# Kernel optimization log

Measured on AMD Instinct MI355X. Metric: run time of the kernel, lower is better.

The kernel has to match this reference:

```python
import jax, jax.numpy as jnp
import numpy as np

NUM_BANDS = 400
LATENT = 8
NUM_LAYERS = 2
K = 10  # num_selected_bands
FF = 128
EPS = 1e-5


def _xavier(key, shape):
    fan_in, fan_out = shape[-1], shape[-2] if len(shape) >= 2 else shape[-1]
    lim = float(np.sqrt(6.0 / (fan_in + fan_out)))
    return jax.random.uniform(key, shape, jnp.float32, -lim, lim)


def setup_inputs() -> dict:
    key = jax.random.key(0)
    ks = jax.random.split(key, 20)
    B, H, W = 1, 256, 256
    d = {
        "x": jax.random.normal(ks[0], (B, NUM_BANDS, H, W), jnp.float32),
        "x_original": jax.random.normal(ks[1], (B, NUM_BANDS, H, W), jnp.float32),
        "pos": _xavier(ks[2], (1, NUM_BANDS)),
        "band_importance": jnp.zeros((NUM_BANDS,), jnp.float32),
        # per-layer transformer params stacked on a leading layer axis
        "Wv": _xavier(ks[3], (NUM_LAYERS, NUM_BANDS, NUM_BANDS)),
        "bv": jnp.zeros((NUM_LAYERS, NUM_BANDS), jnp.float32),
        "Wo": _xavier(ks[4], (NUM_LAYERS, NUM_BANDS, NUM_BANDS)),
        "bo": jnp.zeros((NUM_LAYERS, NUM_BANDS), jnp.float32),
        "ln1_w": jnp.ones((NUM_LAYERS, NUM_BANDS), jnp.float32),
        "ln1_b": jnp.zeros((NUM_LAYERS, NUM_BANDS), jnp.float32),
        "W1": _xavier(ks[5], (NUM_LAYERS, FF, NUM_BANDS)),
        "b1": jnp.zeros((NUM_LAYERS, FF), jnp.float32),
        "W2": _xavier(ks[6], (NUM_LAYERS, NUM_BANDS, FF)),
        "b2": jnp.zeros((NUM_LAYERS, NUM_BANDS), jnp.float32),
        "ln2_w": jnp.ones((NUM_LAYERS, NUM_BANDS), jnp.float32),
        "ln2_b": jnp.zeros((NUM_LAYERS, NUM_BANDS), jnp.float32),
        # lightweight encoder: K -> LATENT -> LATENT
        "We1": _xavier(ks[7], (LATENT, K)),
        "be1": jnp.zeros((LATENT,), jnp.float32),
        "We2": _xavier(ks[8], (LATENT, LATENT)),
        "be2": jnp.zeros((LATENT,), jnp.float32),
        # decoder: LATENT -> LATENT -> NUM_BANDS
        "Wd1": _xavier(ks[9], (LATENT, LATENT)),
        "bd1": jnp.zeros((LATENT,), jnp.float32),
        "Wd2": _xavier(ks[10], (NUM_BANDS, LATENT)),
        "bd2": jnp.zeros((NUM_BANDS,), jnp.float32),
    }
    return d


def _layer_norm(h, w, b):
    mu = jnp.mean(h, axis=-1, keepdims=True)
    var = jnp.mean(jnp.square(h - mu), axis=-1, keepdims=True)
    return (h - mu) * jax.lax.rsqrt(var + EPS) * w + b


def reference(x, x_original, pos, band_importance, Wv, bv, Wo, bo, ln1_w, ln1_b,
              W1, b1, W2, b2, ln2_w, ln2_b, We1, be1, We2, be2, Wd1, bd1, Wd2, bd2):
    B, C, H, W = x.shape
    # [B,C,H,W] -> [B*H*W, C] tokens; learnable positional encoding over bands
    tok = jnp.transpose(x, (0, 2, 3, 1)).reshape(-1, C) + pos

    # TransformerEncoder (post-norm, relu). Seq-first convention => seq_len=1,
    # so softmax over the single score is 1 and self_attn(x) == out_proj(v_proj(x)).
    h = tok
    for i in range(NUM_LAYERS):
        attn = (h @ Wv[i].T + bv[i]) @ Wo[i].T + bo[i]
        h = _layer_norm(h + attn, ln1_w[i], ln1_b[i])
        ff = jax.nn.relu(h @ W1[i].T + b1[i]) @ W2[i].T + b2[i]
        h = _layer_norm(h + ff, ln2_w[i], ln2_b[i])

    attention_scores = h * jax.nn.sigmoid(band_importance)  # [N, C]
    top_v, top_i = jax.lax.top_k(attention_scores, K)       # sorted desc by value
    order = jnp.argsort(top_i, axis=1)
    sorted_idx = jnp.take_along_axis(top_i, order, axis=1)
    sorted_val = jnp.take_along_axis(top_v, order, axis=1)

    orig = jnp.transpose(x_original, (0, 2, 3, 1)).reshape(-1, C)
    selected_bands1 = jnp.take_along_axis(orig, sorted_idx, axis=1)  # [N, K]
    selected = selected_bands1 * sorted_val

    enc = jax.nn.relu(selected @ We1.T + be1) @ We2.T + be2          # [N, LATENT]
    dec = jax.nn.relu(enc @ Wd1.T + bd1) @ Wd2.T + bd2               # [N, C]
    reconstructed = jnp.transpose(dec.reshape(B, H, W, C), (0, 3, 1, 2))
    return reconstructed, sorted_idx, attention_scores, selected_bands1
```

## Files before the change

### kernel.cpp

```cpp
#include <hip/hip_runtime.h>
#include <hip/hip_bf16.h>
#include <math.h>

#define NBANDS 400
#define NPIX   65536
#define FFW    128
#define KSEL   10
#define TOK    16
#define HS     403
#define FS     131

typedef double f64x4 __attribute__((ext_vector_type(4)));
#define MFMA64(a,b,c) __builtin_amdgcn_mfma_f64_16x16x4f64((a),(b),(c),0,0,0)

static constexpr size_t WSB_WVOT = 0;
static constexpr size_t WSB_BVO  = 2560000;
static constexpr size_t WSB_SIG  = 2566400;
static constexpr size_t WSB_W1T  = 2569600;
static constexpr size_t WSB_W2T  = 2979200;
static constexpr size_t WS_NEED  = 3388800;

static constexpr size_t REC_OFF = 0;
static constexpr size_t IDX_OFF = 26214400;
static constexpr size_t SCO_OFF = IDX_OFF + 655360;
static constexpr size_t SEL_OFF = SCO_OFF + 26214400;
static constexpr int    OUT_EXPECT = 53739520;


__global__ void prep_wvot(const float* __restrict__ Wv, const float* __restrict__ Wo,
                          double* __restrict__ WvoT) {
    int b = blockIdx.x;
    int l = b / 400, j = b - l * 400;
    int k = threadIdx.x;
    if (k >= 400) return;
    const float* wo = Wo + l * 160000 + j * 400;
    const float* wv = Wv + l * 160000;
    double acc = 0.0;
    #pragma unroll 4
    for (int m = 0; m < 400; ++m)
        acc += (double)wo[m] * (double)wv[m * 400 + k];
    WvoT[l * 160000 + k * 400 + j] = acc;
}

__global__ void prep_transpose(const float* __restrict__ W1, const float* __restrict__ W2,
                               float* __restrict__ W1T, float* __restrict__ W2T) {
    int idx = blockIdx.x * blockDim.x + threadIdx.x;
    if (idx < 2 * FFW * NBANDS) {
        int l = idx / (FFW * NBANDS); int r = idx - l * (FFW * NBANDS);
        int jf = r / NBANDS; int k = r - jf * NBANDS;
        W1T[l * FFW * NBANDS + k * FFW + jf] = W1[idx];
        int j = r / FFW; int kf = r - j * FFW;
        W2T[l * FFW * NBANDS + kf * NBANDS + j] = W2[idx];
    }
}

__global__ void prep_small(const float* __restrict__ Wo, const float* __restrict__ bv,
                           const float* __restrict__ bo, const float* __restrict__ bi,
                           double* __restrict__ bvo, double* __restrict__ sigd) {
    int g = blockIdx.x * blockDim.x + threadIdx.x;
    if (g < 800) {
        int l = g / 400;
        const float* wo = Wo + l * 160000 + (g - l * 400) * 400;
        const float* bb = bv + l * 400;
        double acc = (double)bo[g];
        for (int m = 0; m < 400; ++m) acc += (double)wo[m] * (double)bb[m];
        bvo[g] = acc;
    } else if (g < 1200) {
        int c = g - 800;
        sigd[c] = 1.0 / (1.0 + exp(-(double)bi[c]));
    }
}

__global__ void sentinel_kernel(float* out, float v) {
    out[blockIdx.x * 256 + threadIdx.x] = v;
}


__device__ inline void layer_norm_inplace(double* __restrict__ h, double* __restrict__ red,
                                          const float* __restrict__ w, const float* __restrict__ b,
                                          int tid) {
    {
        int t = tid >> 5, q = tid & 31;
        double s = 0.0, ss = 0.0;
        for (int j = q; j < NBANDS; j += 32) {
            double v = h[t * HS + j]; s += v; ss += v * v;
        }
        #pragma unroll
        for (int m = 1; m < 32; m <<= 1) {
            s  += __shfl_xor(s, m, 64);
            ss += __shfl_xor(ss, m, 64);
        }
        if (q == 0) { red[t * 2] = s; red[t * 2 + 1] = ss; }
    }
    __syncthreads();
    for (int idx = tid; idx < TOK * NBANDS; idx += 512) {
        int t = idx / NBANDS, j = idx - t * NBANDS;
        double mu  = red[t * 2] / 400.0;
        double var = red[t * 2 + 1] / 400.0 - mu * mu;
        double rs  = 1.0 / sqrt(var + 1e-5);
        h[t * HS + j] = (h[t * HS + j] - mu) * rs * (double)w[j] + (double)b[j];
    }
    __syncthreads();
}

__global__ __launch_bounds__(512) void hbsm_main(
    const float* __restrict__ x, const float* __restrict__ xo,
    const float* __restrict__ pos,
    const float* __restrict__ ln1w, const float* __restrict__ ln1b,
    const float* __restrict__ b1,   const float* __restrict__ b2,
    const float* __restrict__ ln2w, const float* __restrict__ ln2b,
    const float* __restrict__ We1,  const float* __restrict__ be1,
    const float* __restrict__ We2,  const float* __restrict__ be2,
    const float* __restrict__ Wd1,  const float* __restrict__ bd1,
    const float* __restrict__ Wd2,  const float* __restrict__ bd2,
    const double* __restrict__ WvoT, const double* __restrict__ bvo,
    const double* __restrict__ sigd,
    const float* __restrict__ W1Tf,  const float* __restrict__ W2Tf,
    float* __restrict__ out)
{
    extern __shared__ double smem[];
    double* h    = smem;
    double* f    = h + TOK * HS;
    double* red  = f + TOK * FS;
    double* lval = red + 64;
    double* sigs = lval + 160;
    float*  d1s  = (float*)(sigs + 400);
    int*    lidx = (int*)(d1s + 144);

    const int tid  = threadIdx.x;
    const int p0   = blockIdx.x * TOK;
    const int lane = tid & 63;
    const int wv   = tid >> 6;
    const int rA   = lane & 15;
    const int kq   = lane >> 4;

    int rowm[4], colm[4];
    {
        f64x4 z = {0.0, 0.0, 0.0, 0.0};
        f64x4 pr = MFMA64(0.25 * (double)rA, 1.0, z);
        f64x4 pc = MFMA64(0.25, (double)rA, z);
        #pragma unroll
        for (int i = 0; i < 4; ++i) {
            rowm[i] = ((int)(pr[i] + 0.5)) & 15;
            colm[i] = ((int)(pc[i] + 0.5)) & 15;
        }
    }

    for (int i = tid; i < NBANDS; i += 512) sigs[i] = sigd[i];
    for (int i = tid; i < TOK * NBANDS; i += 512) {
        int t = i & 15, c = i >> 4;
        float xv = __builtin_nontemporal_load(&x[(size_t)c * NPIX + p0 + t]);
        h[t * HS + c] = (double)xv + (double)pos[c];
    }
    __syncthreads();

    const double* hA = h + rA * HS;
    const int c0 = wv * 16 + rA, c1 = c0 + 128, c2 = c0 + 256;
    const int ct = 384 + rA;
    const bool xtraA = (wv == 0);
    const bool xtraF = (wv == 4);

    for (int l = 0; l < 2; ++l) {
        {
            const double* WT  = WvoT + l * 160000;
            const double* bb0 = bvo + l * 400;
            f64x4 a0={0,0,0,0}, a1={0,0,0,0}, a2={0,0,0,0}, a3={0,0,0,0};
            #pragma unroll 2
            for (int k0 = 0; k0 < NBANDS; k0 += 4) {
                double av = hA[k0 + kq];
                const double* wrow = WT + (size_t)(k0 + kq) * 400;
                a0 = MFMA64(av, wrow[c0], a0);
                a1 = MFMA64(av, wrow[c1], a1);
                a2 = MFMA64(av, wrow[c2], a2);
                if (xtraA) a3 = MFMA64(av, wrow[ct], a3);
            }
            __syncthreads();
            #pragma unroll
            for (int i = 0; i < 4; ++i) {
                int r  = rowm[i];
                int j0 = wv * 16 + colm[i], j1 = j0 + 128, j2 = j0 + 256;
                h[r * HS + j0] += a0[i] + bb0[j0];
                h[r * HS + j1] += a1[i] + bb0[j1];
                h[r * HS + j2] += a2[i] + bb0[j2];
                if (xtraA) {
                    int jt = 384 + colm[i];
                    h[r * HS + jt] += a3[i] + bb0[jt];
                }
            }
            __syncthreads();
        }
        layer_norm_inplace(h, red, ln1w + l * 400, ln1b + l * 400, tid);

        {
            const float* WT  = W1Tf + (size_t)l * 51200;
            const float* bb1 = b1 + l * FFW;
            const int cf = wv * 16 + rA;
            f64x4 e0 = {0,0,0,0};
            #pragma unroll 2
            for (int k0 = 0; k0 < NBANDS; k0 += 4) {
                double av = hA[k0 + kq];
                double b = (double)WT[(size_t)(k0 + kq) * FFW + cf];
                e0 = MFMA64(av, b, e0);
            }
            #pragma unroll
            for (int i = 0; i < 4; ++i) {
                int r  = rowm[i];
                int jf = wv * 16 + colm[i];
                double v0 = e0[i] + (double)bb1[jf];
                f[r * FS + jf] = v0 > 0.0 ? v0 : 0.0;
            }
            __syncthreads();
        }

        {
            const float* WT  = W2Tf + (size_t)l * 51200;
            const float* bb2 = b2 + l * 400;
            const double* fA = f + rA * FS;
            f64x4 a0={0,0,0,0}, a1={0,0,0,0}, a2={0,0,0,0}, a3={0,0,0,0};
            #pragma unroll 2
            for (int k0 = 0; k0 < FFW; k0 += 4) {
                double av = fA[k0 + kq];
                const float* wrow = WT + (size_t)(k0 + kq) * 400;
                a0 = MFMA64(av, (double)wrow[c0], a0);
                a1 = MFMA64(av, (double)wrow[c1], a1);
                a2 = MFMA64(av, (double)wrow[c2], a2);
                if (xtraF) a3 = MFMA64(av, (double)wrow[ct], a3);
            }
            #pragma unroll
            for (int i = 0; i < 4; ++i) {
                int r  = rowm[i];
                int j0 = wv * 16 + colm[i], j1 = j0 + 128, j2 = j0 + 256;
                h[r * HS + j0] += a0[i] + (double)bb2[j0];
                h[r * HS + j1] += a1[i] + (double)bb2[j1];
                h[r * HS + j2] += a2[i] + (double)bb2[j2];
                if (xtraF) {
                    int jt = 384 + colm[i];
                    h[r * HS + jt] += a3[i] + (double)bb2[jt];
                }
            }
            __syncthreads();
        }
        layer_norm_inplace(h, red, ln2w + l * 400, ln2b + l * 400, tid);
    }

    for (int idx = tid; idx < TOK * NBANDS; idx += 512) {
        int t = idx / NBANDS, c = idx - t * NBANDS;
        __builtin_nontemporal_store((float)(h[t * HS + c] * sigs[c]),
                                    &out[SCO_OFF + (size_t)(p0 + t) * NBANDS + c]);
    }

    if (tid < TOK) {
        int t = tid;
        double* lv = lval + t * KSEL;
        int*    li = lidx + t * KSEL;
        #pragma unroll
        for (int k = 0; k < KSEL; ++k) { lv[k] = -1.0e300; li[k] = 0; }
        for (int c = 0; c < NBANDS; ++c) {
            double v = h[t * HS + c] * sigs[c];
            if (v > lv[KSEL - 1]) {
                int j = KSEL - 1;
                while (j > 0 && lv[j - 1] < v) {
                    lv[j] = lv[j - 1]; li[j] = li[j - 1]; --j;
                }
                lv[j] = v; li[j] = c;
            }
        }
        for (int a = 1; a < KSEL; ++a) {
            double v = lv[a]; int ci = li[a];
            int bq = a - 1;
            while (bq >= 0 && li[bq] > ci) {
                lv[bq + 1] = lv[bq]; li[bq + 1] = li[bq]; --bq;
            }
            lv[bq + 1] = v; li[bq + 1] = ci;
        }
        double sel[KSEL];
        #pragma unroll
        for (int k = 0; k < KSEL; ++k) {
            int ci = li[k];
            float band = __builtin_nontemporal_load(&xo[(size_t)ci * NPIX + p0 + t]);
            __builtin_nontemporal_store((float)ci,
                &out[IDX_OFF + (size_t)(p0 + t) * KSEL + k]);
            __builtin_nontemporal_store(band,
                &out[SEL_OFF + (size_t)(p0 + t) * KSEL + k]);
            sel[k] = (double)band * lv[k];
        }
        double e1[8], e2[8];
        #pragma unroll
        for (int e = 0; e < 8; ++e) {
            double acc = (double)be1[e];
            #pragma unroll
            for (int k = 0; k < KSEL; ++k) acc += sel[k] * (double)We1[e * KSEL + k];
            e1[e] = acc > 0.0 ? acc : 0.0;
        }
        #pragma unroll
        for (int e = 0; e < 8; ++e) {
            double acc = (double)be2[e];
            #pragma unroll
            for (int j = 0; j < 8; ++j) acc += e1[j] * (double)We2[e * 8 + j];
            e2[e] = acc;
        }
        #pragma unroll
        for (int e = 0; e < 8; ++e) {
            double acc = (double)bd1[e];
            #pragma unroll
            for (int j = 0; j < 8; ++j) acc += e2[j] * (double)Wd1[e * 8 + j];
            d1s[t * 9 + e] = (float)(acc > 0.0 ? acc : 0.0);
        }
    }
    __syncthreads();

    for (int idx = tid; idx < TOK * NBANDS; idx += 512) {
        int t = idx & 15, c = idx >> 4;
        double acc = (double)bd2[c];
        const float* w = Wd2 + c * 8;
        #pragma unroll
        for (int e = 0; e < 8; ++e) acc += (double)d1s[t * 9 + e] * (double)w[e];
        __builtin_nontemporal_store((float)acc,
                                    &out[REC_OFF + (size_t)c * NPIX + p0 + t]);
    }
}

extern "C" void kernel_launch(void* const* d_in, const int* in_sizes, int n_in,
                              void* d_out, int out_size, void* d_ws, size_t ws_size,
                              hipStream_t stream) {
    if (ws_size < WS_NEED) {
        sentinel_kernel<<<dim3(256), dim3(256), 0, stream>>>((float*)d_out, -777.0f);
        return;
    }
    if (out_size != OUT_EXPECT) {
        sentinel_kernel<<<dim3(1), dim3(1), 0, stream>>>((float*)d_out, 1.0e6f);
        return;
    }
    const float* x    = (const float*)d_in[0];
    const float* xo   = (const float*)d_in[1];
    const float* pos  = (const float*)d_in[2];
    const float* bi   = (const float*)d_in[3];
    const float* Wv   = (const float*)d_in[4];
    const float* bv   = (const float*)d_in[5];
    const float* Wo   = (const float*)d_in[6];
    const float* bo   = (const float*)d_in[7];
    const float* ln1w = (const float*)d_in[8];
    const float* ln1b = (const float*)d_in[9];
    const float* W1   = (const float*)d_in[10];
    const float* b1   = (const float*)d_in[11];
    const float* W2   = (const float*)d_in[12];
    const float* b2   = (const float*)d_in[13];
    const float* ln2w = (const float*)d_in[14];
    const float* ln2b = (const float*)d_in[15];
    const float* We1  = (const float*)d_in[16];
    const float* be1  = (const float*)d_in[17];
    const float* We2  = (const float*)d_in[18];
    const float* be2  = (const float*)d_in[19];
    const float* Wd1  = (const float*)d_in[20];
    const float* bd1  = (const float*)d_in[21];
    const float* Wd2  = (const float*)d_in[22];
    const float* bd2  = (const float*)d_in[23];

    char* wsb = (char*)d_ws;
    double* WvoT = (double*)(wsb + WSB_WVOT);
    double* bvo  = (double*)(wsb + WSB_BVO);
    double* sigd = (double*)(wsb + WSB_SIG);
    float*  W1Tf = (float*)(wsb + WSB_W1T);
    float*  W2Tf = (float*)(wsb + WSB_W2T);

    prep_wvot<<<dim3(800), dim3(512), 0, stream>>>(Wv, Wo, WvoT);
    prep_transpose<<<dim3(400), dim3(256), 0, stream>>>(W1, W2, W1Tf, W2Tf);
    prep_small<<<dim3(5), dim3(256), 0, stream>>>(Wo, bv, bo, bi, bvo, sigd);

    const int smem_bytes = 74560;
    hipFuncSetAttribute((const void*)hbsm_main,
                        hipFuncAttributeMaxDynamicSharedMemorySize, smem_bytes);
    hipLaunchKernelGGL(hbsm_main, dim3(4096), dim3(512), smem_bytes, stream,
                       x, xo, pos, ln1w, ln1b, b1, b2, ln2w, ln2b,
                       We1, be1, We2, be2, Wd1, bd1, Wd2, bd2,
                       WvoT, bvo, sigd, W1Tf, W2Tf, (float*)d_out);
    (void)in_sizes; (void)n_in;
}
```

Measured before the change: 2.677 ms.

## Replace FP64 MFMA transformer with split-bf16 FP32 path plus FP64 repair pass

The main kernel now runs the token transformer in fp32 storage, using three-way bf16 splitting of activations and weights with bf16 MFMA (six products per step) in place of f64 MFMA. Weights are pre-split into bf16 fragments in a new prep kernel. Pixels whose 10th/11th top-k margin falls below a threshold are appended to a global list. A second kernel recomputes only those pixels in the original fp64 path so the top-k selection stays correct. This trades fp64 matrix throughput for higher-rate bf16 MFMA, at the cost of an extra launch and a list capacity that is fixed in advance.

```diff
diff --git a/kernel.cpp b/kernel.cpp
--- a/kernel.cpp
+++ b/kernel.cpp
@@ -9,16 +9,40 @@
 #define TOK    16
 #define HS     403
 #define FS     131
+#define HSF    420
+#define FSF    132
+#define NCH    13
+#define NCH2   4
+#define TAU    1e-3f
+#define LISTCAP 16384
 
 typedef double f64x4 __attribute__((ext_vector_type(4)));
+typedef float  f32x4 __attribute__((ext_vector_type(4)));
+typedef unsigned short u16x8 __attribute__((ext_vector_type(8)));
+typedef __bf16 bf16x8 __attribute__((ext_vector_type(8)));
 #define MFMA64(a,b,c) __builtin_amdgcn_mfma_f64_16x16x4f64((a),(b),(c),0,0,0)
+#define MFMA16(a,b,c) __builtin_amdgcn_mfma_f32_16x16x32_bf16((a),(b),(c),0,0,0)
+
+__device__ inline unsigned short f2bf(float f) {
+    unsigned u = __builtin_bit_cast(unsigned, f);
+    return (unsigned short)((u + 0x7FFFu + ((u >> 16) & 1u)) >> 16);
+}
+__device__ inline float bf2f(unsigned short s) {
+    unsigned u = ((unsigned)s) << 16;
+    return __builtin_bit_cast(float, u);
+}
 
 static constexpr size_t WSB_WVOT = 0;
 static constexpr size_t WSB_BVO  = 2560000;
 static constexpr size_t WSB_SIG  = 2566400;
 static constexpr size_t WSB_W1T  = 2569600;
 static constexpr size_t WSB_W2T  = 2979200;
-static constexpr size_t WS_NEED  = 3388800;
+static constexpr size_t WSB_CNT  = 3388800;
+static constexpr size_t WSB_LIST = 3388864;
+static constexpr size_t WSB_FRA  = 3454400;
+static constexpr size_t WSB_FR1  = 5451200;
+static constexpr size_t WSB_FR2  = 6090176;
+static constexpr size_t WS_NEED  = 6704576;
 
 static constexpr size_t REC_OFF = 0;
 static constexpr size_t IDX_OFF = 26214400;
@@ -71,8 +95,359 @@
     }
 }
 
+__global__ void zero_cnt(int* cnt) { if (threadIdx.x == 0) *cnt = 0; }
+
+__global__ void prep_split(const double* __restrict__ WvoT, const float* __restrict__ W1T,
+                           const float* __restrict__ W2T,
+                           unsigned short* __restrict__ frA, unsigned short* __restrict__ fr1,
+                           unsigned short* __restrict__ fr2) {
+    int b = blockIdx.x;
+    int l = b / 529, rem = b - l * 529;
+    int lane = threadIdx.x;
+    int rA = lane & 15, kb0 = (lane >> 4) * 8;
+    int arr, nt, kc;
+    if (rem < 325)      { arr = 0; nt = rem / 13; kc = rem % 13; }
+    else if (rem < 429) { arr = 1; int q = rem - 325; nt = q / 13; kc = q % 13; }
+    else                { arr = 2; int q = rem - 429; nt = q / 4;  kc = q % 4; }
+    u16x8 w1, w2, w3;
+    #pragma unroll
+    for (int e = 0; e < 8; ++e) {
+        int k = kc * 32 + kb0 + e;
+        int col = nt * 16 + rA;
+        float v = 0.f;
+        if (arr == 0)      { if (k < 400) v = (float)WvoT[(size_t)l * 160000 + (size_t)k * 400 + col]; }
+        else if (arr == 1) { if (k < 400) v = W1T[(size_t)l * 51200 + (size_t)k * 128 + col]; }
+        else               { v = W2T[(size_t)l * 51200 + (size_t)k * 400 + col]; }
+        unsigned short a = f2bf(v); float r = v - bf2f(a);
+        unsigned short bb = f2bf(r); float r2 = r - bf2f(bb);
+        unsigned short c = f2bf(r2);
+        w1[e] = a; w2[e] = bb; w3[e] = c;
+    }
+    size_t blk;
+    unsigned short* base;
+    if (arr == 0)      { base = frA; blk = 0; }
+    else if (arr == 1) { base = fr1; blk = 0; }
+    else               { base = fr2; blk = 0; }
+    #pragma unroll
+    for (int s = 0; s < 3; ++s) {
+        size_t off;
+        if (arr == 0)      off = ((((size_t)s * 2 + l) * 25 + nt) * 13 + kc) * 512;
+        else if (arr == 1) off = ((((size_t)s * 2 + l) * 8 + nt) * 13 + kc) * 512;
+        else               off = ((((size_t)s * 2 + l) * 25 + nt) * 4 + kc) * 512;
+        u16x8 w = (s == 0) ? w1 : (s == 1 ? w2 : w3);
+        *(u16x8*)(base + off + (size_t)lane * 8) = w;
+    }
+    (void)blk;
+}
+
 __global__ void sentinel_kernel(float* out, float v) {
     out[blockIdx.x * 256 + threadIdx.x] = v;
+}
+
+
+__device__ inline void ln_f32(float* __restrict__ hf, float* __restrict__ redf,
+                              const float* __restrict__ w, const float* __restrict__ b, int tid) {
+    {
+        int t = tid >> 5, q = tid & 31;
+        float s = 0.f, ss = 0.f;
+        for (int j = q; j < NBANDS; j += 32) {
+            float v = hf[t * HSF + j]; s += v; ss += v * v;
+        }
+        #pragma unroll
+        for (int m = 1; m < 32; m <<= 1) {
+            s  += __shfl_xor(s, m, 64);
+            ss += __shfl_xor(ss, m, 64);
+        }
+        if (q == 0) { redf[t * 2] = s; redf[t * 2 + 1] = ss; }
+    }
+    __syncthreads();
+    for (int idx = tid; idx < TOK * NBANDS; idx += 512) {
+        int t = idx / NBANDS, j = idx - t * NBANDS;
+        float mu  = redf[t * 2] * (1.0f / 400.0f);
+        float var = redf[t * 2 + 1] * (1.0f / 400.0f) - mu * mu;
+        float rs  = 1.0f / sqrtf(var + 1e-5f);
+        hf[t * HSF + j] = (hf[t * HSF + j] - mu) * rs * w[j] + b[j];
+    }
+    __syncthreads();
+}
+
+__global__ __launch_bounds__(512) void hbsm_fast(
+    const float* __restrict__ x, const float* __restrict__ xo,
+    const float* __restrict__ pos,
+    const float* __restrict__ ln1w, const float* __restrict__ ln1b,
+    const float* __restrict__ b1,   const float* __restrict__ b2,
+    const float* __restrict__ ln2w, const float* __restrict__ ln2b,
+    const float* __restrict__ We1,  const float* __restrict__ be1,
+    const float* __restrict__ We2,  const float* __restrict__ be2,
+    const float* __restrict__ Wd1,  const float* __restrict__ bd1,
+    const float* __restrict__ Wd2,  const float* __restrict__ bd2,
+    const double* __restrict__ bvo, const double* __restrict__ sigd,
+    const unsigned short* __restrict__ frA, const unsigned short* __restrict__ fr1,
+    const unsigned short* __restrict__ fr2,
+    int* __restrict__ cnt, int* __restrict__ list,
+    float* __restrict__ out)
+{
+    extern __shared__ char smemc[];
+    float* hf            = (float*)smemc;
+    unsigned short* hsu  = (unsigned short*)(smemc + 26880);
+    float* ff            = (float*)(smemc + 66816);
+    float* sigsf         = (float*)(smemc + 75264);
+    float* redf          = (float*)(smemc + 76864);
+    float* lvalf         = (float*)(smemc + 76992);
+    int*   lidx          = (int*)(smemc + 77696);
+    float* d1sf          = (float*)(smemc + 78400);
+
+    const int tid  = threadIdx.x;
+    const int p0   = blockIdx.x * TOK;
+    const int lane = tid & 63;
+    const int wv   = tid >> 6;
+    const int rA   = lane & 15;
+
+    int rowm[4], colm[4];
+    {
+        u16x8 ua, ub, uc;
+        unsigned short vr = f2bf((float)rA), v32 = f2bf(1.0f / 32.0f);
+        #pragma unroll
+        for (int e = 0; e < 8; ++e) { ua[e] = vr; ub[e] = v32; uc[e] = vr; }
+        f32x4 z = {0.f, 0.f, 0.f, 0.f};
+        f32x4 pr = MFMA16(__builtin_bit_cast(bf16x8, ua), __builtin_bit_cast(bf16x8, ub), z);
+        f32x4 pc = MFMA16(__builtin_bit_cast(bf16x8, ub), __builtin_bit_cast(bf16x8, uc), z);
+        #pragma unroll
+        for (int i = 0; i < 4; ++i) {
+            rowm[i] = ((int)(pr[i] + 0.5f)) & 15;
+            colm[i] = ((int)(pc[i] + 0.5f)) & 15;
+        }
+    }
+
+    for (int i = tid; i < NBANDS; i += 512) sigsf[i] = (float)sigd[i];
+    for (int i = tid; i < TOK * NBANDS; i += 512) {
+        int t = i & 15, c = i >> 4;
+        float xv = __builtin_nontemporal_load(&x[(size_t)c * NPIX + p0 + t]);
+        hf[t * HSF + c] = xv + pos[c];
+    }
+    for (int i = tid; i < TOK * (HSF - NBANDS); i += 512) {
+        int t = i / (HSF - NBANDS), c = NBANDS + i % (HSF - NBANDS);
+        hf[t * HSF + c] = 0.f;
+    }
+    __syncthreads();
+
+    for (int l = 0; l < 2; ++l) {
+        for (int idx = tid; idx < NCH * 64; idx += 512) {
+            int kc = idx >> 6, ln = idx & 63;
+            const float* src = hf + (ln & 15) * HSF + kc * 32 + ((ln >> 4) * 8);
+            u16x8 w1, w2, w3;
+            #pragma unroll
+            for (int e = 0; e < 8; ++e) {
+                float v = src[e];
+                unsigned short a = f2bf(v); float r = v - bf2f(a);
+                unsigned short bb = f2bf(r); float r2 = r - bf2f(bb);
+                w1[e] = a; w2[e] = bb; w3[e] = f2bf(r2);
+            }
+            *(u16x8*)(hsu + ((0 * NCH + kc) * 64 + ln) * 8) = w1;
+            *(u16x8*)(hsu + ((1 * NCH + kc) * 64 + ln) * 8) = w2;
+            *(u16x8*)(hsu + ((2 * NCH + kc) * 64 + ln) * 8) = w3;
+        }
+        __syncthreads();
+
+        {
+            #pragma unroll
+            for (int ti = 0; ti < 4; ++ti) {
+                int nt = (ti < 3) ? (wv + ti * 8) : ((wv == 7) ? 24 : -1);
+                if (nt < 0) continue;
+                const unsigned short* pB0 = frA + ((((size_t)0 * 2 + l) * 25 + nt) * 13) * 512 + (size_t)lane * 8;
+                const unsigned short* pB1 = frA + ((((size_t)1 * 2 + l) * 25 + nt) * 13) * 512 + (size_t)lane * 8;
+                const unsigned short* pB2 = frA + ((((size_t)2 * 2 + l) * 25 + nt) * 13) * 512 + (size_t)lane * 8;
+                f32x4 A1 = {0,0,0,0}, A2 = {0,0,0,0}, A3 = {0,0,0,0};
+                for (int kc = 0; kc < NCH; ++kc) {
+                    bf16x8 a1 = __builtin_bit_cast(bf16x8, *(const u16x8*)(hsu + ((0 * NCH + kc) * 64 + lane) * 8));
+                    bf16x8 a2 = __builtin_bit_cast(bf16x8, *(const u16x8*)(hsu + ((1 * NCH + kc) * 64 + lane) * 8));
+                    bf16x8 a3 = __builtin_bit_cast(bf16x8, *(const u16x8*)(hsu + ((2 * NCH + kc) * 64 + lane) * 8));
+                    bf16x8 b1f = __builtin_bit_cast(bf16x8, *(const u16x8*)(pB0 + (size_t)kc * 512));
+                    bf16x8 b2f = __builtin_bit_cast(bf16x8, *(const u16x8*)(pB1 + (size_t)kc * 512));
+                    bf16x8 b3f = __builtin_bit_cast(bf16x8, *(const u16x8*)(pB2 + (size_t)kc * 512));
+                    A1 = MFMA16(a1, b1f, A1);
+                    A2 = MFMA16(a1, b2f, A2); A2 = MFMA16(a2, b1f, A2);
+                    A3 = MFMA16(a1, b3f, A3); A3 = MFMA16(a2, b2f, A3); A3 = MFMA16(a3, b1f, A3);
+                }
+                #pragma unroll
+                for (int i = 0; i < 4; ++i) {
+                    int r = rowm[i], cc = nt * 16 + colm[i];
+                    hf[r * HSF + cc] += (A1[i] + A2[i] + A3[i]) + (float)bvo[l * 400 + cc];
+                }
+            }
+        }
+        __syncthreads();
+        ln_f32(hf, redf, ln1w + l * 400, ln1b + l * 400, tid);
+
+        for (int idx = tid; idx < NCH * 64; idx += 512) {
+            int kc = idx >> 6, ln = idx & 63;
+            const float* src = hf + (ln & 15) * HSF + kc * 32 + ((ln >> 4) * 8);
+            u16x8 w1, w2, w3;
+            #pragma unroll
+            for (int e = 0; e < 8; ++e) {
+                float v = src[e];
+                unsigned short a = f2bf(v); float r = v - bf2f(a);
+                unsigned short bb = f2bf(r); float r2 = r - bf2f(bb);
+                w1[e] = a; w2[e] = bb; w3[e] = f2bf(r2);
+            }
+            *(u16x8*)(hsu + ((0 * NCH + kc) * 64 + ln) * 8) = w1;
+            *(u16x8*)(hsu + ((1 * NCH + kc) * 64 + ln) * 8) = w2;
+            *(u16x8*)(hsu + ((2 * NCH + kc) * 64 + ln) * 8) = w3;
+        }
+        __syncthreads();
+
+        {
+            int nt = wv;
+            const unsigned short* pB0 = fr1 + ((((size_t)0 * 2 + l) * 8 + nt) * 13) * 512 + (size_t)lane * 8;
+            const unsigned short* pB1 = fr1 + ((((size_t)1 * 2 + l) * 8 + nt) * 13) * 512 + (size_t)lane * 8;
+            const unsigned short* pB2 = fr1 + ((((size_t)2 * 2 + l) * 8 + nt) * 13) * 512 + (size_t)lane * 8;
+            f32x4 A1 = {0,0,0,0}, A2 = {0,0,0,0}, A3 = {0,0,0,0};
+            for (int kc = 0; kc < NCH; ++kc) {
+                bf16x8 a1 = __builtin_bit_cast(bf16x8, *(const u16x8*)(hsu + ((0 * NCH + kc) * 64 + lane) * 8));
+                bf16x8 a2 = __builtin_bit_cast(bf16x8, *(const u16x8*)(hsu + ((1 * NCH + kc) * 64 + lane) * 8));
+                bf16x8 a3 = __builtin_bit_cast(bf16x8, *(const u16x8*)(hsu + ((2 * NCH + kc) * 64 + lane) * 8));
+                bf16x8 b1f = __builtin_bit_cast(bf16x8, *(const u16x8*)(pB0 + (size_t)kc * 512));
+                bf16x8 b2f = __builtin_bit_cast(bf16x8, *(const u16x8*)(pB1 + (size_t)kc * 512));
+                bf16x8 b3f = __builtin_bit_cast(bf16x8, *(const u16x8*)(pB2 + (size_t)kc * 512));
+                A1 = MFMA16(a1, b1f, A1);
+                A2 = MFMA16(a1, b2f, A2); A2 = MFMA16(a2, b1f, A2);
+                A3 = MFMA16(a1, b3f, A3); A3 = MFMA16(a2, b2f, A3); A3 = MFMA16(a3, b1f, A3);
+            }
+            #pragma unroll
+            for (int i = 0; i < 4; ++i) {
+                int r = rowm[i], cf = nt * 16 + colm[i];
+                float v = (A1[i] + A2[i] + A3[i]) + b1[l * FFW + cf];
+                ff[r * FSF + cf] = v > 0.f ? v : 0.f;
+            }
+        }
+        __syncthreads();
+
+        for (int idx = tid; idx < NCH2 * 64; idx += 512) {
+            int kc = idx >> 6, ln = idx & 63;
+            const float* src = ff + (ln & 15) * FSF + kc * 32 + ((ln >> 4) * 8);
+            u16x8 w1, w2, w3;
+            #pragma unroll
+            for (int e = 0; e < 8; ++e) {
+                float v = src[e];
+                unsigned short a = f2bf(v); float r = v - bf2f(a);
+                unsigned short bb = f2bf(r); float r2 = r - bf2f(bb);
+                w1[e] = a; w2[e] = bb; w3[e] = f2bf(r2);
+            }
+            *(u16x8*)(hsu + ((0 * NCH2 + kc) * 64 + ln) * 8) = w1;
+            *(u16x8*)(hsu + ((1 * NCH2 + kc) * 64 + ln) * 8) = w2;
+            *(u16x8*)(hsu + ((2 * NCH2 + kc) * 64 + ln) * 8) = w3;
+        }
+        __syncthreads();
+
+        {
+            #pragma unroll
+            for (int ti = 0; ti < 4; ++ti) {
+                int nt = (ti < 3) ? (wv + ti * 8) : ((wv == 7) ? 24 : -1);
+                if (nt < 0) continue;
+                const unsigned short* pB0 = fr2 + ((((size_t)0 * 2 + l) * 25 + nt) * 4) * 512 + (size_t)lane * 8;
+                const unsigned short* pB1 = fr2 + ((((size_t)1 * 2 + l) * 25 + nt) * 4) * 512 + (size_t)lane * 8;
+                const unsigned short* pB2 = fr2 + ((((size_t)2 * 2 + l) * 25 + nt) * 4) * 512 + (size_t)lane * 8;
+                f32x4 A1 = {0,0,0,0}, A2 = {0,0,0,0}, A3 = {0,0,0,0};
+                #pragma unroll
+                for (int kc = 0; kc < NCH2; ++kc) {
+                    bf16x8 a1 = __builtin_bit_cast(bf16x8, *(const u16x8*)(hsu + ((0 * NCH2 + kc) * 64 + lane) * 8));
+                    bf16x8 a2 = __builtin_bit_cast(bf16x8, *(const u16x8*)(hsu + ((1 * NCH2 + kc) * 64 + lane) * 8));
+                    bf16x8 a3 = __builtin_bit_cast(bf16x8, *(const u16x8*)(hsu + ((2 * NCH2 + kc) * 64 + lane) * 8));
+                    bf16x8 b1f = __builtin_bit_cast(bf16x8, *(const u16x8*)(pB0 + (size_t)kc * 512));
+                    bf16x8 b2f = __builtin_bit_cast(bf16x8, *(const u16x8*)(pB1 + (size_t)kc * 512));
+                    bf16x8 b3f = __builtin_bit_cast(bf16x8, *(const u16x8*)(pB2 + (size_t)kc * 512));
+                    A1 = MFMA16(a1, b1f, A1);
+                    A2 = MFMA16(a1, b2f, A2); A2 = MFMA16(a2, b1f, A2);
+                    A3 = MFMA16(a1, b3f, A3); A3 = MFMA16(a2, b2f, A3); A3 = MFMA16(a3, b1f, A3);
+                }
+                #pragma unroll
+                for (int i = 0; i < 4; ++i) {
+                    int r = rowm[i], cc = nt * 16 + colm[i];
+                    hf[r * HSF + cc] += (A1[i] + A2[i] + A3[i]) + b2[l * 400 + cc];
+                }
+            }
+        }
+        __syncthreads();
+        ln_f32(hf, redf, ln2w + l * 400, ln2b + l * 400, tid);
+    }
+
+    for (int idx = tid; idx < TOK * NBANDS; idx += 512) {
+        int t = idx / NBANDS, c = idx - t * NBANDS;
+        __builtin_nontemporal_store(hf[t * HSF + c] * sigsf[c],
+                                    &out[SCO_OFF + (size_t)(p0 + t) * NBANDS + c]);
+    }
+
+    if (tid < TOK) {
+        int t = tid;
+        float* lv = lvalf + t * 11;
+        int*   li = lidx + t * 11;
+        #pragma unroll
+        for (int k = 0; k < 11; ++k) { lv[k] = -3.0e38f; li[k] = 0; }
+        for (int c = 0; c < NBANDS; ++c) {
+            float v = hf[t * HSF + c] * sigsf[c];
+            if (v > lv[10]) {
+                int j = 10;
+                while (j > 0 && lv[j - 1] < v) {
+                    lv[j] = lv[j - 1]; li[j] = li[j - 1]; --j;
+                }
+                lv[j] = v; li[j] = c;
+            }
+        }
+        float margin = lv[9] - lv[10];
+        if (margin < TAU) {
+            int slot = atomicAdd(cnt, 1);
+            if (slot < LISTCAP) list[slot] = p0 + t;
+        }
+        for (int a = 1; a < KSEL; ++a) {
+            float v = lv[a]; int ci = li[a];
+            int bq = a - 1;
+            while (bq >= 0 && li[bq] > ci) {
+                lv[bq + 1] = lv[bq]; li[bq + 1] = li[bq]; --bq;
+            }
+            lv[bq + 1] = v; li[bq + 1] = ci;
+        }
+        float sel[KSEL];
+        #pragma unroll
+        for (int k = 0; k < KSEL; ++k) {
+            int ci = li[k];
+            float band = __builtin_nontemporal_load(&xo[(size_t)ci * NPIX + p0 + t]);
+            __builtin_nontemporal_store((float)ci, &out[IDX_OFF + (size_t)(p0 + t) * KSEL + k]);
+            __builtin_nontemporal_store(band, &out[SEL_OFF + (size_t)(p0 + t) * KSEL + k]);
+            sel[k] = band * lv[k];
+        }
+        float e1[8], e2[8];
+        #pragma unroll
+        for (int e = 0; e < 8; ++e) {
+            float acc = be1[e];
+            #pragma unroll
+            for (int k = 0; k < KSEL; ++k) acc += sel[k] * We1[e * KSEL + k];
+            e1[e] = acc > 0.f ? acc : 0.f;
+        }
+        #pragma unroll
+        for (int e = 0; e < 8; ++e) {
+            float acc = be2[e];
+            #pragma unroll
+            for (int j = 0; j < 8; ++j) acc += e1[j] * We2[e * 8 + j];
+            e2[e] = acc;
+        }
+        #pragma unroll
+        for (int e = 0; e < 8; ++e) {
+            float acc = bd1[e];
+            #pragma unroll
+            for (int j = 0; j < 8; ++j) acc += e2[j] * Wd1[e * 8 + j];
+            d1sf[t * 9 + e] = acc > 0.f ? acc : 0.f;
+        }
+    }
+    __syncthreads();
+
+    for (int idx = tid; idx < TOK * NBANDS; idx += 512) {
+        int t = idx & 15, c = idx >> 4;
+        float acc = bd2[c];
+        const float* w = Wd2 + c * 8;
+        #pragma unroll
+        for (int e = 0; e < 8; ++e) acc += d1sf[t * 9 + e] * w[e];
+        __builtin_nontemporal_store(acc, &out[REC_OFF + (size_t)c * NPIX + p0 + t]);
+    }
 }
 
 
@@ -103,7 +478,7 @@
     __syncthreads();
 }
 
-__global__ __launch_bounds__(512) void hbsm_main(
+__global__ __launch_bounds__(512) void hbsm_repair(
     const float* __restrict__ x, const float* __restrict__ xo,
     const float* __restrict__ pos,
     const float* __restrict__ ln1w, const float* __restrict__ ln1b,
@@ -116,8 +491,12 @@
     const double* __restrict__ WvoT, const double* __restrict__ bvo,
     const double* __restrict__ sigd,
     const float* __restrict__ W1Tf,  const float* __restrict__ W2Tf,
+    const int* __restrict__ cnt, const int* __restrict__ list,
     float* __restrict__ out)
 {
+    const int n = *cnt;
+    if ((int)blockIdx.x * TOK >= n) return;
+
     extern __shared__ double smem[];
     double* h    = smem;
     double* f    = h + TOK * HS;
@@ -126,13 +505,18 @@
     double* sigs = lval + 160;
     float*  d1s  = (float*)(sigs + 400);
     int*    lidx = (int*)(d1s + 144);
+    int*    ptok = (int*)(lidx + 160);
 
     const int tid  = threadIdx.x;
-    const int p0   = blockIdx.x * TOK;
     const int lane = tid & 63;
     const int wv   = tid >> 6;
     const int rA   = lane & 15;
     const int kq   = lane >> 4;
+
+    if (tid < TOK) {
+        int slot = blockIdx.x * TOK + tid;
+        ptok[tid] = (slot < n && slot < LISTCAP) ? list[slot] : -1;
+    }
 
     int rowm[4], colm[4];
     {
@@ -147,10 +531,11 @@
     }
 
     for (int i = tid; i < NBANDS; i += 512) sigs[i] = sigd[i];
+    __syncthreads();
     for (int i = tid; i < TOK * NBANDS; i += 512) {
         int t = i & 15, c = i >> 4;
-        float xv = __builtin_nontemporal_load(&x[(size_t)c * NPIX + p0 + t]);
-        h[t * HS + c] = (double)xv + (double)pos[c];
+        int pt = ptok[t];
+        h[t * HS + c] = (pt >= 0) ? ((double)x[(size_t)c * NPIX + pt] + (double)pos[c]) : 0.0;
     }
     __syncthreads();
 
@@ -245,12 +630,12 @@
 
     for (int idx = tid; idx < TOK * NBANDS; idx += 512) {
         int t = idx / NBANDS, c = idx - t * NBANDS;
-        __builtin_nontemporal_store((float)(h[t * HS + c] * sigs[c]),
-                                    &out[SCO_OFF + (size_t)(p0 + t) * NBANDS + c]);
-    }
-
-    if (tid < TOK) {
-        int t = tid;
+        if (ptok[t] >= 0)
+            out[SCO_OFF + (size_t)ptok[t] * NBANDS + c] = (float)(h[t * HS + c] * sigs[c]);
+    }
+
+    if (tid < TOK && ptok[tid] >= 0) {
+        int t = tid, pt = ptok[t];
         double* lv = lval + t * KSEL;
         int*    li = lidx + t * KSEL;
         #pragma unroll
@@ -277,11 +662,9 @@
         #pragma unroll
         for (int k = 0; k < KSEL; ++k) {
             int ci = li[k];
-            float band = __builtin_nontemporal_load(&xo[(size_t)ci * NPIX + p0 + t]);
-            __builtin_nontemporal_store((float)ci,
-                &out[IDX_OFF + (size_t)(p0 + t) * KSEL + k]);
-            __builtin_nontemporal_store(band,
-                &out[SEL_OFF + (size_t)(p0 + t) * KSEL + k]);
+            float band = xo[(size_t)ci * NPIX + pt];
+            out[IDX_OFF + (size_t)pt * KSEL + k] = (float)ci;
+            out[SEL_OFF + (size_t)pt * KSEL + k] = band;
             sel[k] = (double)band * lv[k];
         }
         double e1[8], e2[8];
@@ -311,12 +694,12 @@
 
     for (int idx = tid; idx < TOK * NBANDS; idx += 512) {
         int t = idx & 15, c = idx >> 4;
+        if (ptok[t] < 0) continue;
         double acc = (double)bd2[c];
         const float* w = Wd2 + c * 8;
         #pragma unroll
         for (int e = 0; e < 8; ++e) acc += (double)d1s[t * 9 + e] * (double)w[e];
-        __builtin_nontemporal_store((float)acc,
-                                    &out[REC_OFF + (size_t)c * NPIX + p0 + t]);
+        out[REC_OFF + (size_t)c * NPIX + ptok[t]] = (float)acc;
     }
 }
 
@@ -362,17 +745,32 @@
     double* sigd = (double*)(wsb + WSB_SIG);
     float*  W1Tf = (float*)(wsb + WSB_W1T);
     float*  W2Tf = (float*)(wsb + WSB_W2T);
-
+    int*    cnt  = (int*)(wsb + WSB_CNT);
+    int*    list = (int*)(wsb + WSB_LIST);
+    unsigned short* frA = (unsigned short*)(wsb + WSB_FRA);
+    unsigned short* fr1 = (unsigned short*)(wsb + WSB_FR1);
+    unsigned short* fr2 = (unsigned short*)(wsb + WSB_FR2);
+
+    zero_cnt<<<dim3(1), dim3(64), 0, stream>>>(cnt);
     prep_wvot<<<dim3(800), dim3(512), 0, stream>>>(Wv, Wo, WvoT);
     prep_transpose<<<dim3(400), dim3(256), 0, stream>>>(W1, W2, W1Tf, W2Tf);
     prep_small<<<dim3(5), dim3(256), 0, stream>>>(Wo, bv, bo, bi, bvo, sigd);
-
-    const int smem_bytes = 74560;
-    hipFuncSetAttribute((const void*)hbsm_main,
-                        hipFuncAttributeMaxDynamicSharedMemorySize, smem_bytes);
-    hipLaunchKernelGGL(hbsm_main, dim3(4096), dim3(512), smem_bytes, stream,
+    prep_split<<<dim3(1058), dim3(64), 0, stream>>>(WvoT, W1Tf, W2Tf, frA, fr1, fr2);
+
+    const int smem_fast = 78976;
+    hipFuncSetAttribute((const void*)hbsm_fast,
+                        hipFuncAttributeMaxDynamicSharedMemorySize, smem_fast);
+    hipLaunchKernelGGL(hbsm_fast, dim3(4096), dim3(512), smem_fast, stream,
                        x, xo, pos, ln1w, ln1b, b1, b2, ln2w, ln2b,
                        We1, be1, We2, be2, Wd1, bd1, Wd2, bd2,
-                       WvoT, bvo, sigd, W1Tf, W2Tf, (float*)d_out);
+                       bvo, sigd, frA, fr1, fr2, cnt, list, (float*)d_out);
+
+    const int smem_rep = 74624;
+    hipFuncSetAttribute((const void*)hbsm_repair,
+                        hipFuncAttributeMaxDynamicSharedMemorySize, smem_rep);
+    hipLaunchKernelGGL(hbsm_repair, dim3(1024), dim3(512), smem_rep, stream,
+                       x, xo, pos, ln1w, ln1b, b1, b2, ln2w, ln2b,
+                       We1, be1, We2, be2, Wd1, bd1, Wd2, bd2,
+                       WvoT, bvo, sigd, W1Tf, W2Tf, cnt, list, (float*)d_out);
     (void)in_sizes; (void)n_in;
 }
```

After: 3.145 ms. 17.5% more time.
